# Kernel tuning notes

Measured on AMD Instinct MI355X. Metric: run time of the kernel, lower is better.

Reference implementation:

```python
import jax, jax.numpy as jnp
import numpy as np
from jax import lax

SOFTPLUS_THRESHOLD = 20.0

def _softplus_thresh(z):
    # softplus(z, beta=1, threshold=20): linear above threshold
    return jnp.where(z > SOFTPLUS_THRESHOLD, z,
                     jnp.log1p(jnp.exp(jnp.minimum(z, SOFTPLUS_THRESHOLD))))

def setup_inputs() -> dict:
    key = jax.random.key(0)
    ks = jax.random.split(key, 8)
    L, E, R, N = 512, 5120, 160, 16
    scale = 0.02
    x = jax.random.normal(ks[0], (1, 1, L, E), dtype=jnp.float32)
    W_dt_low = jax.random.normal(ks[1], (E, R), dtype=jnp.float32) * scale
    W_dt = jax.random.normal(ks[2], (R, E), dtype=jnp.float32) * scale
    dt_bias = jax.random.normal(ks[3], (E,), dtype=jnp.float32) * scale
    W_B = jax.random.normal(ks[4], (E, N), dtype=jnp.float32) * scale
    W_C = jax.random.normal(ks[5], (E, N), dtype=jnp.float32) * scale
    # A_log ~ log of positive values so A = -exp(A_log) is a stable decay
    A_log = jnp.log(1.0 + jax.random.uniform(ks[6], (E, N), dtype=jnp.float32) * 15.0)
    D = jax.random.normal(ks[7], (E,), dtype=jnp.float32)
    return {"x": x, "W_dt_low": W_dt_low, "W_dt": W_dt, "dt_bias": dt_bias,
            "W_B": W_B, "W_C": W_C, "A_log": A_log, "D": D}

def reference(x, W_dt_low, W_dt, dt_bias, W_B, W_C, A_log, D):
    orig_shape = x.shape              # [1,1,L,E]
    L, E = orig_shape[-2], orig_shape[-1]
    xf = x.reshape(L, E)
    # delta_t: x -> dt_rank -> d_inner, then thresholded softplus
    delta = _softplus_thresh((xf @ W_dt_low) @ W_dt + dt_bias)   # [L,E]
    A = -jnp.exp(A_log)                                          # [E,N]
    # discretization: abar = exp(delta * A), bbar = delta * B * x
    abar = jnp.exp(delta[:, :, None] * A[None])                  # [L,E,N]
    B = xf @ W_B                                                 # [L,N]
    bbar = delta[:, :, None] * B[:, None, :] * xf[:, :, None]    # [L,E,N]
    # linear recurrence h_t = abar_t * h_{t-1} + bbar_t via associative scan
    def combine(c1, c2):
        a1, b1 = c1
        a2, b2 = c2
        return a1 * a2, a2 * b1 + b2
    _, h = lax.associative_scan(combine, (abar, bbar), axis=0)   # [L,E,N]
    C = xf @ W_C                                                 # [L,N]
    y = jnp.einsum('len,ln->le', h, C)                           # hc_sum_reduce
    out = xf * D + y
    return out.reshape(orig_shape)
```

## Files before the change

### kernel.cpp

```cpp
#include <hip/hip_runtime.h>
#include <math.h>

#define LL 512
#define EE 5120
#define RR 160
#define NS 16
#define NTOT 192
#define KS 32
#define KCHUNK 160
#define CH 8
#define NC 64

#define XCONV_BLOCKS 1280
#define WALL_TILES   960
#define WDT_TILES    800

typedef __attribute__((ext_vector_type(8))) short short8;
typedef __attribute__((ext_vector_type(4))) short short4v;
typedef __attribute__((ext_vector_type(4))) float f32x4;

__device__ inline float softplus_t(float z) {
    return z > 20.f ? z : log1pf(__expf(fminf(z, 20.f)));
}

__device__ inline short f2bf(float f) {
    unsigned u = __float_as_uint(f);
    unsigned r = (u + 0x7FFFu + ((u >> 16) & 1u)) >> 16;
    return (short)r;
}

__device__ inline float bf2f(unsigned short u) {
    return __uint_as_float(((unsigned)u) << 16);
}

__global__ __launch_bounds__(256) void prep_kernel(
        const float* __restrict__ x,
        const float* __restrict__ Wlow,
        const float* __restrict__ WB,
        const float* __restrict__ WC,
        const float* __restrict__ Wdt,
        short* __restrict__ xb,
        short* __restrict__ WallT,
        short* __restrict__ WdtT) {
    const int tid = threadIdx.x;
    const int bid = blockIdx.x;
    if (bid < XCONV_BLOCKS) {
        size_t base = (size_t)bid * 2048 + (size_t)tid * 8;
        float4 v0 = *reinterpret_cast<const float4*>(x + base);
        float4 v1 = *reinterpret_cast<const float4*>(x + base + 4);
        short8 o;
        o[0] = f2bf(v0.x); o[1] = f2bf(v0.y); o[2] = f2bf(v0.z); o[3] = f2bf(v0.w);
        o[4] = f2bf(v1.x); o[5] = f2bf(v1.y); o[6] = f2bf(v1.z); o[7] = f2bf(v1.w);
        *reinterpret_cast<short8*>(xb + base) = o;
        return;
    }
    __shared__ float tile[32][33];
    const int row = tid >> 3, col4 = (tid & 7) * 4;
    if (bid < XCONV_BLOCKS + WALL_TILES) {
        const int t = bid - XCONV_BLOCKS;
        const int k0 = (t / 6) * 32, n0 = (t % 6) * 32;
#pragma unroll
        for (int i = 0; i < 4; ++i) {
            int n = n0 + col4 + i, k = k0 + row;
            float v;
            if (n < RR)            v = Wlow[(size_t)k * RR + n];
            else if (n < RR + NS)  v = WB[(size_t)k * NS + (n - RR)];
            else                   v = WC[(size_t)k * NS + (n - RR - NS)];
            tile[row][col4 + i] = v;
        }
        __syncthreads();
        const int nr = tid >> 3, kc = (tid & 7) * 4;
        short4v o;
#pragma unroll
        for (int i = 0; i < 4; ++i) o[i] = f2bf(tile[kc + i][nr]);
        *reinterpret_cast<short4v*>(WallT + (size_t)(n0 + nr) * EE + k0 + kc) = o;
    } else {
        const int t = bid - XCONV_BLOCKS - WALL_TILES;
        const int n0 = (t / 5) * 32, k0 = (t % 5) * 32;
#pragma unroll
        for (int i = 0; i < 4; ++i)
            tile[row][col4 + i] = Wdt[(size_t)(k0 + row) * EE + n0 + col4 + i];
        __syncthreads();
        const int nr = tid >> 3, kc = (tid & 7) * 4;
        short4v o;
#pragma unroll
        for (int i = 0; i < 4; ++i) o[i] = f2bf(tile[kc + i][nr]);
        *reinterpret_cast<short4v*>(WdtT + (size_t)(n0 + nr) * RR + k0 + kc) = o;
    }
}

__global__ __launch_bounds__(256) void g1m_kernel(
        const short* __restrict__ xb,
        const short* __restrict__ WallT,
        short* __restrict__ part) {
    const int tid = threadIdx.x;
    const int w = tid >> 6, l = tid & 63;
    const int wm = w >> 1, wn = w & 1;
    const int m0 = blockIdx.x * 64 + wm * 32;
    const int n0 = blockIdx.y * 64 + wn * 32;
    const int kz = blockIdx.z;
    const int row16 = l & 15, kg = (l >> 4) * 8;
    f32x4 acc[2][2] = {};
    const short* ap0 = xb + (size_t)(m0 + row16) * EE + kz * KCHUNK + kg;
    const short* ap1 = ap0 + (size_t)16 * EE;
    const short* bp0 = WallT + (size_t)(n0 + row16) * EE + kz * KCHUNK + kg;
    const short* bp1 = bp0 + (size_t)16 * EE;
#pragma unroll
    for (int s = 0; s < KCHUNK / 32; ++s) {
        short8 a0 = *reinterpret_cast<const short8*>(ap0 + s * 32);
        short8 a1 = *reinterpret_cast<const short8*>(ap1 + s * 32);
        short8 b0 = *reinterpret_cast<const short8*>(bp0 + s * 32);
        short8 b1 = *reinterpret_cast<const short8*>(bp1 + s * 32);
        acc[0][0] = __builtin_amdgcn_mfma_f32_16x16x32_bf16(a0, b0, acc[0][0], 0, 0, 0);
        acc[0][1] = __builtin_amdgcn_mfma_f32_16x16x32_bf16(a0, b1, acc[0][1], 0, 0, 0);
        acc[1][0] = __builtin_amdgcn_mfma_f32_16x16x32_bf16(a1, b0, acc[1][0], 0, 0, 0);
        acc[1][1] = __builtin_amdgcn_mfma_f32_16x16x32_bf16(a1, b1, acc[1][1], 0, 0, 0);
    }
    const int r0 = (l >> 4) * 4;
    const int c = l & 15;
#pragma unroll
    for (int i = 0; i < 2; ++i)
#pragma unroll
        for (int j = 0; j < 2; ++j) {
            size_t base = ((size_t)kz * LL + (m0 + i * 16 + r0)) * NTOT + (n0 + j * 16 + c);
            part[base]            = f2bf(acc[i][j][0]);
            part[base + NTOT]     = f2bf(acc[i][j][1]);
            part[base + 2 * NTOT] = f2bf(acc[i][j][2]);
            part[base + 3 * NTOT] = f2bf(acc[i][j][3]);
        }
}

__global__ __launch_bounds__(256) void r1_kernel(
        const short* __restrict__ part,
        short* __restrict__ tmpb,
        float* __restrict__ Bb,
        float* __restrict__ Cb) {
    int idx = blockIdx.x * 256 + threadIdx.x;
    int m = idx / NTOT, j = idx % NTOT;
    float s = 0.f;
#pragma unroll
    for (int ks = 0; ks < KS; ++ks)
        s += bf2f((unsigned short)part[(size_t)ks * LL * NTOT + idx]);
    if (j < RR) tmpb[m * RR + j] = f2bf(s);
    else if (j < RR + NS) Bb[m * NS + (j - RR)] = s;
    else Cb[m * NS + (j - RR - NS)] = s;
}

__global__ __launch_bounds__(256) void g2m_kernel(
        const short* __restrict__ tmpb,
        const short* __restrict__ WdtT,
        const float* __restrict__ bias,
        unsigned short* __restrict__ deltab) {
    const int tid = threadIdx.x;
    const int w = tid >> 6, l = tid & 63;
    const int wm = w >> 1, wn = w & 1;
    const int m0 = blockIdx.x * 64 + wm * 32;
    const int n0 = blockIdx.y * 64 + wn * 32;
    const int row16 = l & 15, koff = (l >> 4) * 8;
    f32x4 acc[2][2] = {};
    const short* aptr0 = tmpb + (size_t)(m0 + row16) * RR + koff;
    const short* aptr1 = aptr0 + (size_t)16 * RR;
    const short* bptr0 = WdtT + (size_t)(n0 + row16) * RR + koff;
    const short* bptr1 = bptr0 + (size_t)16 * RR;
#pragma unroll
    for (int s = 0; s < 5; ++s) {
        short8 a0 = *reinterpret_cast<const short8*>(aptr0 + s * 32);
        short8 a1 = *reinterpret_cast<const short8*>(aptr1 + s * 32);
        short8 b0 = *reinterpret_cast<const short8*>(bptr0 + s * 32);
        short8 b1 = *reinterpret_cast<const short8*>(bptr1 + s * 32);
        acc[0][0] = __builtin_amdgcn_mfma_f32_16x16x32_bf16(a0, b0, acc[0][0], 0, 0, 0);
        acc[0][1] = __builtin_amdgcn_mfma_f32_16x16x32_bf16(a0, b1, acc[0][1], 0, 0, 0);
        acc[1][0] = __builtin_amdgcn_mfma_f32_16x16x32_bf16(a1, b0, acc[1][0], 0, 0, 0);
        acc[1][1] = __builtin_amdgcn_mfma_f32_16x16x32_bf16(a1, b1, acc[1][1], 0, 0, 0);
    }
    const int r0 = (l >> 4) * 4;
    const int c = l & 15;
#pragma unroll
    for (int i = 0; i < 2; ++i) {
        int m = m0 + i * 16 + r0;
#pragma unroll
        for (int j = 0; j < 2; ++j) {
            int n = n0 + j * 16 + c;
            float bv = bias[n];
#pragma unroll
            for (int r = 0; r < 4; ++r)
                deltab[(size_t)(m + r) * EE + n] =
                    (unsigned short)f2bf(softplus_t(acc[i][j][r] + bv));
        }
    }
}

__global__ __launch_bounds__(256) void passA_kernel(
        const unsigned short* __restrict__ deltab,
        const unsigned short* __restrict__ xb,
        const float* __restrict__ Bb,
        const float* __restrict__ A_log,
        unsigned short* __restrict__ Hloc,
        float* __restrict__ sumd) {
    __shared__ float b_lds[CH][NS];
    const int c = blockIdx.y;
    const int e = blockIdx.x * 256 + threadIdx.x;
    const int t0 = c * CH;
    for (int v = threadIdx.x; v < CH * NS; v += 256)
        b_lds[v >> 4][v & 15] = Bb[t0 * NS + v];
    __syncthreads();

    float Ac[NS];
#pragma unroll
    for (int q = 0; q < 4; ++q) {
        float4 al = *reinterpret_cast<const float4*>(&A_log[(size_t)e * NS + q * 4]);
        Ac[q * 4 + 0] = -__expf(al.x);
        Ac[q * 4 + 1] = -__expf(al.y);
        Ac[q * 4 + 2] = -__expf(al.z);
        Ac[q * 4 + 3] = -__expf(al.w);
    }
    float h[NS];
#pragma unroll
    for (int n = 0; n < NS; ++n) h[n] = 0.f;
    float sd = 0.f;

#pragma unroll
    for (int tt = 0; tt < CH; ++tt) {
        float d  = bf2f(deltab[(size_t)(t0 + tt) * EE + e]);
        float xv = bf2f(xb[(size_t)(t0 + tt) * EE + e]);
        sd += d;
        float bx = d * xv;
#pragma unroll
        for (int n = 0; n < NS; ++n) {
            float a = __expf(d * Ac[n]);
            h[n] = a * h[n] + bx * b_lds[tt][n];
        }
    }
    size_t base = ((size_t)c * EE + e) * NS;
    short8 p0, p1;
#pragma unroll
    for (int n = 0; n < 8; ++n) { p0[n] = f2bf(h[n]); p1[n] = f2bf(h[n + 8]); }
    *reinterpret_cast<short8*>(Hloc + base)     = p0;
    *reinterpret_cast<short8*>(Hloc + base + 8) = p1;
    sumd[(size_t)c * EE + e] = sd;
}

__global__ __launch_bounds__(256) void passB_kernel(
        const unsigned short* __restrict__ Hloc,
        const float* __restrict__ sumd,
        const float* __restrict__ A_log,
        unsigned short* __restrict__ Hstart) {
    const int wk = blockIdx.x * 256 + threadIdx.x;
    const int eB = wk >> 4;
    const float AcB = -__expf(A_log[wk]);
    float hs = 0.f;
#pragma unroll
    for (int cc = 0; cc < NC; ++cc) {
        size_t off = (size_t)cc * EE * NS + wk;
        Hstart[off] = (unsigned short)f2bf(hs);
        hs = __expf(AcB * sumd[(size_t)cc * EE + eB]) * hs + bf2f(Hloc[off]);
    }
}

__global__ __launch_bounds__(256) void passC_kernel(
        const unsigned short* __restrict__ deltab,
        const unsigned short* __restrict__ xb,
        const float* __restrict__ Bb,
        const float* __restrict__ Cb,
        const float* __restrict__ A_log,
        const float* __restrict__ Dvec,
        const unsigned short* __restrict__ Hstart,
        float* __restrict__ out) {
    __shared__ float b_lds[CH][NS];
    __shared__ float c_lds[CH][NS];
    const int c = blockIdx.y;
    const int e = blockIdx.x * 256 + threadIdx.x;
    const int t0 = c * CH;
    for (int v = threadIdx.x; v < CH * NS; v += 256) {
        b_lds[v >> 4][v & 15] = Bb[t0 * NS + v];
        c_lds[v >> 4][v & 15] = Cb[t0 * NS + v];
    }
    __syncthreads();

    float Ac[NS];
#pragma unroll
    for (int q = 0; q < 4; ++q) {
        float4 al = *reinterpret_cast<const float4*>(&A_log[(size_t)e * NS + q * 4]);
        Ac[q * 4 + 0] = -__expf(al.x);
        Ac[q * 4 + 1] = -__expf(al.y);
        Ac[q * 4 + 2] = -__expf(al.z);
        Ac[q * 4 + 3] = -__expf(al.w);
    }
    float h[NS];
    size_t base = ((size_t)c * EE + e) * NS;
    {
        short8 p0 = *reinterpret_cast<const short8*>(Hstart + base);
        short8 p1 = *reinterpret_cast<const short8*>(Hstart + base + 8);
#pragma unroll
        for (int n = 0; n < 8; ++n) {
            h[n]     = bf2f((unsigned short)p0[n]);
            h[n + 8] = bf2f((unsigned short)p1[n]);
        }
    }
    const float Dval = Dvec[e];

#pragma unroll
    for (int tt = 0; tt < CH; ++tt) {
        float d  = bf2f(deltab[(size_t)(t0 + tt) * EE + e]);
        float xv = bf2f(xb[(size_t)(t0 + tt) * EE + e]);
        float bx = d * xv;
        float y = 0.f;
#pragma unroll
        for (int n = 0; n < NS; ++n) {
            float a = __expf(d * Ac[n]);
            h[n] = a * h[n] + bx * b_lds[tt][n];
            y += h[n] * c_lds[tt][n];
        }
        out[(size_t)(t0 + tt) * EE + e] = xv * Dval + y;
    }
}

extern "C" void kernel_launch(void* const* d_in, const int* in_sizes, int n_in,
                              void* d_out, int out_size, void* d_ws, size_t ws_size,
                              hipStream_t stream) {
    const float* x     = (const float*)d_in[0];
    const float* Wlow  = (const float*)d_in[1];
    const float* Wdt   = (const float*)d_in[2];
    const float* bias  = (const float*)d_in[3];
    const float* WB    = (const float*)d_in[4];
    const float* WC    = (const float*)d_in[5];
    const float* Alog  = (const float*)d_in[6];
    const float* Dv    = (const float*)d_in[7];
    float* out = (float*)d_out;
    float* wsf = (float*)d_ws;

    float*          Bb     = wsf;
    float*          Cb     = wsf + 8192;
    short*          WallT  = (short*)(wsf + 16384);
    short*          WdtT   = (short*)(wsf + 507904);
    short*          tmpb   = (short*)(wsf + 917504);
    short*          xb     = (short*)(wsf + 958464);
    short*          part   = (short*)(wsf + 2269184);
    unsigned short* deltab = (unsigned short*)(wsf + 3842048);
    unsigned short* Hloc   = (unsigned short*)(wsf + 5152768);
    unsigned short* Hstart = (unsigned short*)(wsf + 7774208);
    float*          sumd   = wsf + 10395648;

    prep_kernel<<<dim3(XCONV_BLOCKS + WALL_TILES + WDT_TILES), 256, 0, stream>>>(
        x, Wlow, WB, WC, Wdt, xb, WallT, WdtT);
    g1m_kernel<<<dim3(8, 3, KS), 256, 0, stream>>>(xb, WallT, part);
    r1_kernel<<<dim3(384), 256, 0, stream>>>(part, tmpb, Bb, Cb);
    g2m_kernel<<<dim3(8, 80), 256, 0, stream>>>(tmpb, WdtT, bias, deltab);
    passA_kernel<<<dim3(EE / 256, NC), 256, 0, stream>>>(
        deltab, (const unsigned short*)xb, Bb, Alog, Hloc, sumd);
    passB_kernel<<<dim3((EE * NS) / 256), 256, 0, stream>>>(Hloc, sumd, Alog, Hstart);
    passC_kernel<<<dim3(EE / 256, NC), 256, 0, stream>>>(
        deltab, (const unsigned short*)xb, Bb, Cb, Alog, Dv, Hstart, out);
}
```

Baseline: 70.77 us.

## Fuse split-K reduction into GEMM1 and delta GEMM into scan pass A

Removes the separate split-K reduction kernel: the last block per output tile, found through an atomic counter, sums the partials in place. Moves the second low-rank GEMM plus softplus into the first scan pass, so delta is computed into LDS per chunk and written out for pass C. Doubles the scan chunk length (CH 16, NC 32) to match the 16-row MFMA tile and halve the carry count. This saves two launches and a full round trip of delta through memory, but adds a serial tail on the last-arriving blocks and reduces scan parallelism.

```diff
diff --git a/kernel.cpp b/kernel.cpp
--- a/kernel.cpp
+++ b/kernel.cpp
@@ -8,12 +8,13 @@
 #define NTOT 192
 #define KS 32
 #define KCHUNK 160
-#define CH 8
-#define NC 64
+#define CH 16
+#define NC 32
 
 #define XCONV_BLOCKS 1280
 #define WALL_TILES   960
 #define WDT_TILES    800
+#define NTILES 24
 
 typedef __attribute__((ext_vector_type(8))) short short8;
 typedef __attribute__((ext_vector_type(4))) short short4v;
@@ -41,10 +42,12 @@
         const float* __restrict__ Wdt,
         short* __restrict__ xb,
         short* __restrict__ WallT,
-        short* __restrict__ WdtT) {
+        short* __restrict__ WdtT,
+        int* __restrict__ counters) {
     const int tid = threadIdx.x;
     const int bid = blockIdx.x;
     if (bid < XCONV_BLOCKS) {
+        if (bid == 0 && tid < NTILES) counters[tid] = 0;
         size_t base = (size_t)bid * 2048 + (size_t)tid * 8;
         float4 v0 = *reinterpret_cast<const float4*>(x + base);
         float4 v1 = *reinterpret_cast<const float4*>(x + base + 4);
@@ -92,12 +95,17 @@
 __global__ __launch_bounds__(256) void g1m_kernel(
         const short* __restrict__ xb,
         const short* __restrict__ WallT,
-        short* __restrict__ part) {
+        short* __restrict__ part,
+        int* __restrict__ counters,
+        short* __restrict__ tmpb,
+        float* __restrict__ Bb,
+        float* __restrict__ Cb) {
     const int tid = threadIdx.x;
     const int w = tid >> 6, l = tid & 63;
     const int wm = w >> 1, wn = w & 1;
-    const int m0 = blockIdx.x * 64 + wm * 32;
-    const int n0 = blockIdx.y * 64 + wn * 32;
+    const int m0b = blockIdx.x * 64, n0b = blockIdx.y * 64;
+    const int m0 = m0b + wm * 32;
+    const int n0 = n0b + wn * 32;
     const int kz = blockIdx.z;
     const int row16 = l & 15, kg = (l >> 4) * 8;
     f32x4 acc[2][2] = {};
@@ -128,83 +136,79 @@
             part[base + 2 * NTOT] = f2bf(acc[i][j][2]);
             part[base + 3 * NTOT] = f2bf(acc[i][j][3]);
         }
-}
-
-__global__ __launch_bounds__(256) void r1_kernel(
-        const short* __restrict__ part,
-        short* __restrict__ tmpb,
-        float* __restrict__ Bb,
-        float* __restrict__ Cb) {
-    int idx = blockIdx.x * 256 + threadIdx.x;
-    int m = idx / NTOT, j = idx % NTOT;
-    float s = 0.f;
-#pragma unroll
-    for (int ks = 0; ks < KS; ++ks)
-        s += bf2f((unsigned short)part[(size_t)ks * LL * NTOT + idx]);
-    if (j < RR) tmpb[m * RR + j] = f2bf(s);
-    else if (j < RR + NS) Bb[m * NS + (j - RR)] = s;
-    else Cb[m * NS + (j - RR - NS)] = s;
-}
-
-__global__ __launch_bounds__(256) void g2m_kernel(
+
+    __threadfence();
+    __shared__ int is_last;
+    if (tid == 0) {
+        int prev = atomicAdd(&counters[blockIdx.x * 3 + blockIdx.y], 1);
+        is_last = (prev == KS - 1) ? 1 : 0;
+    }
+    __syncthreads();
+    if (!is_last) return;
+    __threadfence();
+#pragma unroll
+    for (int k = 0; k < 16; ++k) {
+        int v = tid + k * 256;
+        int mr = v >> 6, nc = v & 63;
+        int m = m0b + mr, j = n0b + nc;
+        float s = 0.f;
+#pragma unroll 8
+        for (int ks = 0; ks < KS; ++ks)
+            s += bf2f((unsigned short)part[((size_t)ks * LL + m) * NTOT + j]);
+        if (j < RR) tmpb[m * RR + j] = f2bf(s);
+        else if (j < RR + NS) Bb[m * NS + (j - RR)] = s;
+        else Cb[m * NS + (j - RR - NS)] = s;
+    }
+}
+
+__global__ __launch_bounds__(256) void passAf_kernel(
         const short* __restrict__ tmpb,
         const short* __restrict__ WdtT,
         const float* __restrict__ bias,
-        unsigned short* __restrict__ deltab) {
-    const int tid = threadIdx.x;
-    const int w = tid >> 6, l = tid & 63;
-    const int wm = w >> 1, wn = w & 1;
-    const int m0 = blockIdx.x * 64 + wm * 32;
-    const int n0 = blockIdx.y * 64 + wn * 32;
-    const int row16 = l & 15, koff = (l >> 4) * 8;
-    f32x4 acc[2][2] = {};
-    const short* aptr0 = tmpb + (size_t)(m0 + row16) * RR + koff;
-    const short* aptr1 = aptr0 + (size_t)16 * RR;
-    const short* bptr0 = WdtT + (size_t)(n0 + row16) * RR + koff;
-    const short* bptr1 = bptr0 + (size_t)16 * RR;
-#pragma unroll
-    for (int s = 0; s < 5; ++s) {
-        short8 a0 = *reinterpret_cast<const short8*>(aptr0 + s * 32);
-        short8 a1 = *reinterpret_cast<const short8*>(aptr1 + s * 32);
-        short8 b0 = *reinterpret_cast<const short8*>(bptr0 + s * 32);
-        short8 b1 = *reinterpret_cast<const short8*>(bptr1 + s * 32);
-        acc[0][0] = __builtin_amdgcn_mfma_f32_16x16x32_bf16(a0, b0, acc[0][0], 0, 0, 0);
-        acc[0][1] = __builtin_amdgcn_mfma_f32_16x16x32_bf16(a0, b1, acc[0][1], 0, 0, 0);
-        acc[1][0] = __builtin_amdgcn_mfma_f32_16x16x32_bf16(a1, b0, acc[1][0], 0, 0, 0);
-        acc[1][1] = __builtin_amdgcn_mfma_f32_16x16x32_bf16(a1, b1, acc[1][1], 0, 0, 0);
-    }
-    const int r0 = (l >> 4) * 4;
-    const int c = l & 15;
-#pragma unroll
-    for (int i = 0; i < 2; ++i) {
-        int m = m0 + i * 16 + r0;
-#pragma unroll
-        for (int j = 0; j < 2; ++j) {
-            int n = n0 + j * 16 + c;
-            float bv = bias[n];
-#pragma unroll
-            for (int r = 0; r < 4; ++r)
-                deltab[(size_t)(m + r) * EE + n] =
-                    (unsigned short)f2bf(softplus_t(acc[i][j][r] + bv));
-        }
-    }
-}
-
-__global__ __launch_bounds__(256) void passA_kernel(
-        const unsigned short* __restrict__ deltab,
         const unsigned short* __restrict__ xb,
         const float* __restrict__ Bb,
         const float* __restrict__ A_log,
+        unsigned short* __restrict__ deltab,
         unsigned short* __restrict__ Hloc,
         float* __restrict__ sumd) {
+    __shared__ float d_lds[CH][257];
     __shared__ float b_lds[CH][NS];
     const int c = blockIdx.y;
-    const int e = blockIdx.x * 256 + threadIdx.x;
+    const int e0 = blockIdx.x * 256;
+    const int tid = threadIdx.x;
     const int t0 = c * CH;
-    for (int v = threadIdx.x; v < CH * NS; v += 256)
-        b_lds[v >> 4][v & 15] = Bb[t0 * NS + v];
+    const int w = tid >> 6, l = tid & 63;
+
+    b_lds[tid >> 4][tid & 15] = Bb[t0 * NS + tid];
+
+    {
+        const int row16 = l & 15, koff = (l >> 4) * 8;
+        f32x4 acc[4] = {};
+        const short* bp = tmpb + (size_t)(t0 + row16) * RR + koff;
+        const short* ap = WdtT + (size_t)(e0 + w * 64 + row16) * RR + koff;
+#pragma unroll
+        for (int s = 0; s < 5; ++s) {
+            short8 b0 = *reinterpret_cast<const short8*>(bp + s * 32);
+#pragma unroll
+            for (int ef = 0; ef < 4; ++ef) {
+                short8 a0 = *reinterpret_cast<const short8*>(ap + (size_t)ef * 16 * RR + s * 32);
+                acc[ef] = __builtin_amdgcn_mfma_f32_16x16x32_bf16(a0, b0, acc[ef], 0, 0, 0);
+            }
+        }
+        const int r0 = (l >> 4) * 4, tl = l & 15;
+#pragma unroll
+        for (int ef = 0; ef < 4; ++ef) {
+#pragma unroll
+            for (int r = 0; r < 4; ++r) {
+                int el = w * 64 + ef * 16 + r0 + r;
+                float dv = softplus_t(acc[ef][r] + bias[e0 + el]);
+                d_lds[tl][el] = bf2f((unsigned short)f2bf(dv));
+            }
+        }
+    }
     __syncthreads();
 
+    const int e = e0 + tid;
     float Ac[NS];
 #pragma unroll
     for (int q = 0; q < 4; ++q) {
@@ -221,7 +225,8 @@
 
 #pragma unroll
     for (int tt = 0; tt < CH; ++tt) {
-        float d  = bf2f(deltab[(size_t)(t0 + tt) * EE + e]);
+        float d = d_lds[tt][tid];
+        deltab[(size_t)(t0 + tt) * EE + e] = (unsigned short)f2bf(d);
         float xv = bf2f(xb[(size_t)(t0 + tt) * EE + e]);
         sd += d;
         float bx = d * xv;
@@ -338,17 +343,18 @@
     short*          part   = (short*)(wsf + 2269184);
     unsigned short* deltab = (unsigned short*)(wsf + 3842048);
     unsigned short* Hloc   = (unsigned short*)(wsf + 5152768);
-    unsigned short* Hstart = (unsigned short*)(wsf + 7774208);
-    float*          sumd   = wsf + 10395648;
+    unsigned short* Hstart = (unsigned short*)(wsf + 6463488);
+    float*          sumd   = wsf + 7774208;
+    int*            counters = (int*)(wsf + 7938048);
 
     prep_kernel<<<dim3(XCONV_BLOCKS + WALL_TILES + WDT_TILES), 256, 0, stream>>>(
-        x, Wlow, WB, WC, Wdt, xb, WallT, WdtT);
-    g1m_kernel<<<dim3(8, 3, KS), 256, 0, stream>>>(xb, WallT, part);
-    r1_kernel<<<dim3(384), 256, 0, stream>>>(part, tmpb, Bb, Cb);
-    g2m_kernel<<<dim3(8, 80), 256, 0, stream>>>(tmpb, WdtT, bias, deltab);
-    passA_kernel<<<dim3(EE / 256, NC), 256, 0, stream>>>(
-        deltab, (const unsigned short*)xb, Bb, Alog, Hloc, sumd);
+        x, Wlow, WB, WC, Wdt, xb, WallT, WdtT, counters);
+    g1m_kernel<<<dim3(8, 3, KS), 256, 0, stream>>>(
+        xb, WallT, part, counters, tmpb, Bb, Cb);
+    passAf_kernel<<<dim3(EE / 256, NC), 256, 0, stream>>>(
+        tmpb, WdtT, bias, (const unsigned short*)xb, Bb, Alog, deltab, Hloc, sumd);
     passB_kernel<<<dim3((EE * NS) / 256), 256, 0, stream>>>(Hloc, sumd, Alog, Hstart);
     passC_kernel<<<dim3(EE / 256, NC), 256, 0, stream>>>(
-        deltab, (const unsigned short*)xb, Bb, Cb, Alog, Dv, Hstart, out);
-}
+        (const unsigned short*)deltab, (const unsigned short*)xb, Bb, Cb, Alog, Dv,
+        Hstart, out);
+}
```

Measured after the change: 184.9 us. 161% more time.
